# Optimization experiments

Hardware: AMD Instinct MI355X
Metric: run time of the kernel (lower is better)

The kernel has to match this reference:

```python
import jax, jax.numpy as jnp
import numpy as np
from jax import lax

R = 3
D = (2 * R + 1) ** 2  # 49 local offsets


def _unfold(x, r):
    # torch F.unfold(kernel=2r+1, padding=r): (B,C,H,W) -> (B, C*K*K, H, W),
    # channel-major (c, ky, kx) ordering, matching conv_general_dilated_patches.
    k = 2 * r + 1
    return lax.conv_general_dilated_patches(
        x, (k, k), (1, 1), [(r, r), (r, r)],
        dimension_numbers=("NCHW", "OIHW", "NCHW"))


def _l2norm(x, eps=1e-12):
    n = jnp.sqrt(jnp.sum(x * x, axis=1, keepdims=True))
    return x / jnp.maximum(n, eps)


def setup_inputs() -> dict:
    key = jax.random.key(0)
    ks = jax.random.split(key, 8)
    B, Cin, Cmid, H, W = 2, 256, 128, 112, 112
    phi_cur = jax.random.normal(ks[0], (B, Cin, H, W), jnp.float32)
    phi_rnd = jax.random.normal(ks[1], (B, Cin, H, W), jnp.float32)
    P_cur = jax.random.normal(ks[2], (B, 3, H, W), jnp.float32)
    P_rnd = jax.random.normal(ks[3], (B, 3, H, W), jnp.float32)
    Wq = jax.random.normal(ks[4], (Cmid, Cin), jnp.float32) * 0.05
    Wk = jax.random.normal(ks[5], (Cmid, Cin), jnp.float32) * 0.05
    Wv = jax.random.normal(ks[6], (D, D), jnp.float32) * 0.1
    bv = jnp.zeros((D,), jnp.float32)
    gamma = jnp.array(1.0, jnp.float32)
    return dict(phi_cur=phi_cur, phi_rnd=phi_rnd, P_cur=P_cur, P_rnd=P_rnd,
                Wq=Wq, Wk=Wk, Wv=Wv, bv=bv, gamma=gamma)


def reference(phi_cur, phi_rnd, P_cur, P_rnd, Wq, Wk, Wv, bv, gamma):
    B, _, H, W = phi_cur.shape
    # 1x1 convs + channel L2 normalize
    q = _l2norm(jnp.einsum('oc,bchw->bohw', Wq, phi_cur))
    k = _l2norm(jnp.einsum('oc,bchw->bohw', Wk, phi_rnd))
    # local cost volume: patches (B, Cmid, D, H, W)
    patches = _unfold(k, R).reshape(B, -1, D, H, W)
    corr = jnp.einsum('bchw,bcdhw->bdhw', q, patches)  # (B,D,H,W)
    vol_corr = jnp.einsum('ed,bdhw->behw', Wv, corr) + bv[None, :, None, None]
    # geometric bias
    Pr = _unfold(P_rnd, R).reshape(B, 3, D, H, W)
    dP = P_cur[:, :, None, :, :] - Pr  # (B,3,D,H,W)
    dz = dP[:, 2]
    dist = jnp.sqrt(jnp.clip(jnp.sum(dP * dP, axis=1), 1e-12, None))
    logits = vol_corr + gamma * (-dist - 0.5 * jnp.abs(dz))
    w = jax.nn.softmax(logits, axis=1)
    off = jnp.arange(-R, R + 1, dtype=w.dtype)
    dY, dX = jnp.meshgrid(off, off, indexing='ij')
    offx = dX.reshape(1, D, 1, 1)
    offy = dY.reshape(1, D, 1, 1)
    du = jnp.sum(w * offx, axis=1, keepdims=True)
    dv = jnp.sum(w * offy, axis=1, keepdims=True)
    conf = jnp.max(w, axis=1, keepdims=True)
    return du, dv, conf
```

## Files before the change

### kernel.cpp

```cpp
#include <hip/hip_runtime.h>
#include <hip/hip_bf16.h>
#include <math.h>

constexpr int B    = 2;
constexpr int CIN  = 256;
constexpr int CMID = 128;
constexpr int H    = 112;
constexpr int W    = 112;
constexpr int HW   = H * W;
constexpr int NPIX = B * HW;
constexpr int RAD  = 3;
constexpr int KS   = 7;
constexpr int DD   = 49;

typedef __attribute__((ext_vector_type(8))) short  short8;
typedef __attribute__((ext_vector_type(4))) float  float4v;

__device__ __forceinline__ unsigned pkbf(float a, float b) {
    __hip_bfloat162 h = __float22bfloat162_rn(make_float2(a, b));
    union { __hip_bfloat162 h2; unsigned u; } c;
    c.h2 = h;
    return c.u;
}

__global__ __launch_bounds__(256) void prep(
    const float* __restrict__ Wq, const float* __restrict__ Wk,
    const float* __restrict__ Wv,
    unsigned short* __restrict__ wqb, unsigned short* __restrict__ wkb,
    float* __restrict__ wvp)
{
    if (blockIdx.x < 64) {
        const int i  = blockIdx.x * 256 + threadIdx.x;
        const int n4 = (CMID * CIN) / 4;
        const float4 v = (i < n4) ? ((const float4*)Wq)[i] : ((const float4*)Wk)[i - n4];
        uint2 r;
        r.x = pkbf(v.x, v.y);
        r.y = pkbf(v.z, v.w);
        if (i < n4) ((uint2*)wqb)[i] = r;
        else        ((uint2*)wkb)[i - n4] = r;
    } else {
        for (int idx = threadIdx.x; idx < DD * 52; idx += 256) {
            const int r = idx / 52, c = idx % 52;
            wvp[idx] = (c < DD) ? Wv[r * DD + c] : 0.f;
        }
    }
}

constexpr int PSTR = 264;

__global__ __launch_bounds__(256, 4) void proj_mfma(
    const float* __restrict__ phi_cur, const float* __restrict__ phi_rnd,
    const unsigned short* __restrict__ wq_bf, const unsigned short* __restrict__ wk_bf,
    unsigned short* __restrict__ q_ws, unsigned short* __restrict__ k_ws)
{
    __shared__ unsigned short pt[64 * PSTR];
    __shared__ float red[4][64];

    const int tid  = threadIdx.x;
    const int lane = tid & 63;
    const int wv   = __builtin_amdgcn_readfirstlane(tid >> 6);
    const int t    = blockIdx.y;

    const float* __restrict__ phi          = t ? phi_rnd : phi_cur;
    const unsigned short* __restrict__ Wbf = t ? wk_bf : wq_bf;
    unsigned short* __restrict__ outp      = t ? k_ws : q_ws;

    const int pgb = blockIdx.x * 64;
    const int b   = pgb / HW;
    const int pim = pgb % HW;
    const float* pbase = phi + (size_t)b * CIN * HW + pim;

#pragma unroll
    for (int pass = 0; pass < 8; ++pass) {
        const int idx = pass * 256 + tid;
        const int cp  = idx >> 4;
        const int pq  = idx & 15;
        const int c0  = cp * 2;
        const int swz = ((pq >> 1) & 3) << 3;
        const float4 va = *(const float4*)(pbase + (size_t)c0 * HW + pq * 4);
        const float4 vb = *(const float4*)(pbase + (size_t)(c0 + 1) * HW + pq * 4);
        const int col = c0 ^ swz;
        *(unsigned*)(pt + (pq * 4 + 0) * PSTR + col) = pkbf(va.x, vb.x);
        *(unsigned*)(pt + (pq * 4 + 1) * PSTR + col) = pkbf(va.y, vb.y);
        *(unsigned*)(pt + (pq * 4 + 2) * PSTR + col) = pkbf(va.z, vb.z);
        *(unsigned*)(pt + (pq * 4 + 3) * PSTR + col) = pkbf(va.w, vb.w);
    }

    __syncthreads();

    const int m = lane & 15, quad = lane >> 4;
    float4v acc[2][4];
#pragma unroll
    for (int ot = 0; ot < 2; ++ot)
#pragma unroll
        for (int nt = 0; nt < 4; ++nt) acc[ot][nt] = (float4v)0.f;

#pragma unroll
    for (int kc = 0; kc < 8; ++kc) {
        const short8 af0 = *(const short8*)(Wbf +
            (size_t)(wv * 32 + m) * CIN + kc * 32 + quad * 8);
        const short8 af1 = *(const short8*)(Wbf +
            (size_t)(wv * 32 + 16 + m) * CIN + kc * 32 + quad * 8);
        short8 bfr[4];
#pragma unroll
        for (int nt = 0; nt < 4; ++nt) {
            const int row = nt * 16 + m;
            const int col = (kc * 32 + quad * 8) ^ (((row >> 3) & 3) << 3);
            bfr[nt] = *(const short8*)(pt + row * PSTR + col);
        }
#pragma unroll
        for (int nt = 0; nt < 4; ++nt) {
            acc[0][nt] = __builtin_amdgcn_mfma_f32_16x16x32_bf16(af0, bfr[nt], acc[0][nt], 0, 0, 0);
            acc[1][nt] = __builtin_amdgcn_mfma_f32_16x16x32_bf16(af1, bfr[nt], acc[1][nt], 0, 0, 0);
        }
    }

#pragma unroll
    for (int nt = 0; nt < 4; ++nt) {
        float ss = 0.f;
#pragma unroll
        for (int ot = 0; ot < 2; ++ot)
#pragma unroll
            for (int r = 0; r < 4; ++r)
                ss = fmaf(acc[ot][nt][r], acc[ot][nt][r], ss);
        ss += __shfl_xor(ss, 16, 64);
        ss += __shfl_xor(ss, 32, 64);
        if (quad == 0) red[wv][nt * 16 + m] = ss;
    }
    __syncthreads();

    float inv[4];
#pragma unroll
    for (int nt = 0; nt < 4; ++nt) {
        const int px = nt * 16 + m;
        const float tot = red[0][px] + red[1][px] + red[2][px] + red[3][px];
        inv[nt] = 1.f / fmaxf(sqrtf(tot), 1e-12f);
    }

#pragma unroll
    for (int nt = 0; nt < 4; ++nt)
#pragma unroll
        for (int ot = 0; ot < 2; ++ot) {
            uint2 st;
            st.x = pkbf(acc[ot][nt][0] * inv[nt], acc[ot][nt][1] * inv[nt]);
            st.y = pkbf(acc[ot][nt][2] * inv[nt], acc[ot][nt][3] * inv[nt]);
            *(uint2*)(outp + (size_t)(pgb + nt * 16 + m) * CMID
                      + wv * 32 + ot * 16 + quad * 4) = st;
        }
}

constexpr int TILE = 16;
constexpr int COLS = TILE + 6;
constexpr int NV   = KS * COLS;
constexpr int KSTR = 136;

__global__ __launch_bounds__(256) void corr_kernel(
    const unsigned short* __restrict__ q_ws, const unsigned short* __restrict__ k_ws,
    const float* __restrict__ P_cur, const float* __restrict__ P_rnd,
    const float* __restrict__ wvp, const float* __restrict__ bv,
    const float* __restrict__ gamma_p, float* __restrict__ out)
{
    __shared__ unsigned short kt[NV * KSTR];
    __shared__ alignas(16) unsigned short qt[TILE * KSTR];
    __shared__ float cs[TILE][52];

    const int tid  = threadIdx.x;
    const int lane = tid & 63;
    const int wv   = __builtin_amdgcn_readfirstlane(tid >> 6);

    const int fid = (blockIdx.z * H + blockIdx.y) * (W / TILE) + blockIdx.x;
    const int swz = (fid & 7) * 196 + (fid >> 3);
    const int b   = swz / (H * (W / TILE));
    const int rem = swz % (H * (W / TILE));
    const int h   = rem / (W / TILE);
    const int w0  = (rem % (W / TILE)) * TILE;

    const int sub  = tid & 15;
    const int vgrp = tid >> 4;
#pragma unroll
    for (int pass = 0; pass < 10; ++pass) {
        const int vi = pass * 16 + vgrp;
        if (vi < NV) {
            const int rr = vi / COLS;
            const int cc = vi % COLS;
            const int hh = h + rr - RAD;
            const int ww = w0 + cc - RAD;
            uint4 v = make_uint4(0, 0, 0, 0);
            if (hh >= 0 && hh < H && ww >= 0 && ww < W)
                v = *(const uint4*)(k_ws + (size_t)(b * HW + hh * W + ww) * CMID + sub * 8);
            *(uint4*)(kt + vi * KSTR + sub * 8) = v;
        }
    }
    {
        const uint4 v = *(const uint4*)(q_ws + (size_t)(b * HW + h * W + w0 + vgrp) * CMID + sub * 8);
        *(uint4*)(qt + vgrp * KSTR + sub * 8) = v;
    }

    const int  ld    = (lane < DD) ? lane : 0;
    const bool valid = (lane < DD);
    float4 wq4[13];
#pragma unroll
    for (int j = 0; j < 13; ++j)
        wq4[j] = *(const float4*)(wvp + ld * 52 + j * 4);
    const float bvv   = bv[ld];
    const float gamma = gamma_p[0];

    __syncthreads();

    if (tid < TILE * 3)
        cs[tid / 3][49 + tid % 3] = 0.f;

    const int m = lane & 15, quad = lane >> 4;
    for (int g = wv; g < 14; g += 4) {
        const int r  = g >> 1;
        const int nt = g & 1;
        const int vi = min(r * COLS + nt * 16 + m, NV - 1);
        float4v acc = (float4v)0.f;
#pragma unroll
        for (int kc = 0; kc < 4; ++kc) {
            const short8 afrag = *(const short8*)(qt + m * KSTR + kc * 32 + quad * 8);
            const short8 bfrag = *(const short8*)(kt + vi * KSTR + kc * 32 + quad * 8);
            acc = __builtin_amdgcn_mfma_f32_16x16x32_bf16(afrag, bfrag, acc, 0, 0, 0);
        }
#pragma unroll
        for (int reg = 0; reg < 4; ++reg) {
            const int p   = quad * 4 + reg;
            const int off = nt * 16 + m - p;
            if (off >= 0 && off <= 6)
                cs[p][r * 7 + off] = acc[reg];
        }
    }
    __syncthreads();
    float* lsf = reinterpret_cast<float*>(qt);

    const int dy = ld / KS - RAD;
    const int dx = ld % KS - RAD;

#pragma unroll
    for (int i = 0; i < 4; ++i) {
        const int pl = wv * 4 + i;

        const int hn = h + dy, wn = w0 + pl + dx;
        const bool inb = valid && hn >= 0 && hn < H && wn >= 0 && wn < W;
        const float* pc = P_cur + (size_t)b * 3 * HW + (h * W + w0 + pl);
        const float cx = pc[0], cy = pc[HW], cz = pc[2 * HW];
        float rx = 0.f, ry = 0.f, rz = 0.f;
        if (inb) {
            const float* pr = P_rnd + (size_t)b * 3 * HW + (hn * W + wn);
            rx = pr[0]; ry = pr[HW]; rz = pr[2 * HW];
        }
        const float dpx = cx - rx, dpy = cy - ry, dpz = cz - rz;
        const float dist = sqrtf(fmaxf(dpx * dpx + dpy * dpy + dpz * dpz, 1e-12f));

        float logit = -INFINITY;
        if (valid) {
            float va0 = bvv, va1 = 0.f;
#pragma unroll
            for (int e4 = 0; e4 < 13; ++e4) {
                const float4 c4 = *(const float4*)&cs[pl][e4 * 4];
                const float4 w4 = wq4[e4];
                if (e4 & 1) {
                    va1 = fmaf(w4.x, c4.x, va1);
                    va1 = fmaf(w4.y, c4.y, va1);
                    va1 = fmaf(w4.z, c4.z, va1);
                    va1 = fmaf(w4.w, c4.w, va1);
                } else {
                    va0 = fmaf(w4.x, c4.x, va0);
                    va0 = fmaf(w4.y, c4.y, va0);
                    va0 = fmaf(w4.z, c4.z, va0);
                    va0 = fmaf(w4.w, c4.w, va0);
                }
            }
            logit = (va0 + va1) + gamma * (-dist - 0.5f * fabsf(dpz));
        }
        lsf[pl * 64 + lane] = logit;
    }

    {
        const int pli = lane >> 4;
        const int dq  = lane & 15;
        const int pl  = wv * 4 + pli;

        const float4 v = ((const float4*)lsf)[pl * 16 + dq];

        float m4 = fmaxf(fmaxf(v.x, v.y), fmaxf(v.z, v.w));
#pragma unroll
        for (int s = 1; s < 16; s <<= 1)
            m4 = fmaxf(m4, __shfl_xor(m4, s, 64));

        const float e0 = __expf(v.x - m4);
        const float e1 = __expf(v.y - m4);
        const float e2 = __expf(v.z - m4);
        const float e3 = __expf(v.w - m4);
        float Z = (e0 + e1) + (e2 + e3);

        const int c0i = dq * 4;
        float dus = 0.f, dvs = 0.f;
        {
            const float ex[4] = { e0, e1, e2, e3 };
#pragma unroll
            for (int j = 0; j < 4; ++j) {
                const int col = c0i + j;
                dus = fmaf(ex[j], (float)(col % KS - RAD), dus);
                dvs = fmaf(ex[j], (float)(col / KS - RAD), dvs);
            }
        }
#pragma unroll
        for (int s = 1; s < 16; s <<= 1) {
            Z   += __shfl_xor(Z,   s, 64);
            dus += __shfl_xor(dus, s, 64);
            dvs += __shfl_xor(dvs, s, 64);
        }

        if (dq == 0) {
            const int pg = b * HW + h * W + w0 + pl;
            const float invZ = 1.f / Z;
            out[pg]            = dus * invZ;
            out[NPIX + pg]     = dvs * invZ;
            out[2 * NPIX + pg] = invZ;
        }
    }
}

extern "C" void kernel_launch(void* const* d_in, const int* in_sizes, int n_in,
                              void* d_out, int out_size, void* d_ws, size_t ws_size,
                              hipStream_t stream)
{
    const float* phi_cur = (const float*)d_in[0];
    const float* phi_rnd = (const float*)d_in[1];
    const float* P_cur   = (const float*)d_in[2];
    const float* P_rnd   = (const float*)d_in[3];
    const float* Wq      = (const float*)d_in[4];
    const float* Wk      = (const float*)d_in[5];
    const float* Wv      = (const float*)d_in[6];
    const float* bv      = (const float*)d_in[7];
    const float* gm      = (const float*)d_in[8];
    float* out = (float*)d_out;

    unsigned short* ws   = (unsigned short*)d_ws;
    unsigned short* q_ws = ws;
    unsigned short* k_ws = q_ws + (size_t)NPIX * CMID;
    unsigned short* wqb  = k_ws + (size_t)NPIX * CMID;
    unsigned short* wkb  = wqb + (size_t)CMID * CIN;
    float*          wvp  = (float*)(wkb + (size_t)CMID * CIN);

    prep<<<dim3(65), 256, 0, stream>>>(Wq, Wk, Wv, wqb, wkb, wvp);

    proj_mfma<<<dim3(NPIX / 64, 2), 256, 0, stream>>>(
        phi_cur, phi_rnd, wqb, wkb, q_ws, k_ws);

    corr_kernel<<<dim3(W / TILE, H, B), 256, 0, stream>>>(
        q_ws, k_ws, P_cur, P_rnd, wvp, bv, gm, out);
}
```

Before: 138.4 us.

## Fuse weight prep into projection kernel, halve pixel tile, hoist geometry loads

Removes the separate prep launch: the projection kernel now reads fp32 Wq/Wk directly, converts them to bf16 in registers with a one-step prefetch, and block 0 pads Wv. The projection pixel tile shrinks from 64 to 32 pixels per block, which doubles the block count and changes the LDS swizzle. In the correlation kernel the geometric bias loads and math move ahead of the MFMA phase so their global loads overlap the shared-memory work. The cost is that each block re-reads and re-converts fp32 weights, giving more global weight traffic and conversion ALU per block. Block 0 also writes wvp with no ordering against the next kernel other than stream order.

```diff
diff --git a/kernel.cpp b/kernel.cpp
--- a/kernel.cpp
+++ b/kernel.cpp
@@ -23,60 +23,40 @@
     return c.u;
 }
 
-__global__ __launch_bounds__(256) void prep(
+constexpr int PIX  = 32;
+constexpr int PSTR = 264;
+
+__global__ __launch_bounds__(256, 4) void proj_mfma(
+    const float* __restrict__ phi_cur, const float* __restrict__ phi_rnd,
     const float* __restrict__ Wq, const float* __restrict__ Wk,
     const float* __restrict__ Wv,
-    unsigned short* __restrict__ wqb, unsigned short* __restrict__ wkb,
+    unsigned short* __restrict__ q_ws, unsigned short* __restrict__ k_ws,
     float* __restrict__ wvp)
 {
-    if (blockIdx.x < 64) {
-        const int i  = blockIdx.x * 256 + threadIdx.x;
-        const int n4 = (CMID * CIN) / 4;
-        const float4 v = (i < n4) ? ((const float4*)Wq)[i] : ((const float4*)Wk)[i - n4];
-        uint2 r;
-        r.x = pkbf(v.x, v.y);
-        r.y = pkbf(v.z, v.w);
-        if (i < n4) ((uint2*)wqb)[i] = r;
-        else        ((uint2*)wkb)[i - n4] = r;
-    } else {
-        for (int idx = threadIdx.x; idx < DD * 52; idx += 256) {
-            const int r = idx / 52, c = idx % 52;
-            wvp[idx] = (c < DD) ? Wv[r * DD + c] : 0.f;
-        }
-    }
-}
-
-constexpr int PSTR = 264;
-
-__global__ __launch_bounds__(256, 4) void proj_mfma(
-    const float* __restrict__ phi_cur, const float* __restrict__ phi_rnd,
-    const unsigned short* __restrict__ wq_bf, const unsigned short* __restrict__ wk_bf,
-    unsigned short* __restrict__ q_ws, unsigned short* __restrict__ k_ws)
-{
-    __shared__ unsigned short pt[64 * PSTR];
-    __shared__ float red[4][64];
+    __shared__ unsigned short pt[PIX * PSTR];
+    __shared__ float red[4][PIX];
 
     const int tid  = threadIdx.x;
     const int lane = tid & 63;
     const int wv   = __builtin_amdgcn_readfirstlane(tid >> 6);
     const int t    = blockIdx.y;
 
-    const float* __restrict__ phi          = t ? phi_rnd : phi_cur;
-    const unsigned short* __restrict__ Wbf = t ? wk_bf : wq_bf;
-    unsigned short* __restrict__ outp      = t ? k_ws : q_ws;
-
-    const int pgb = blockIdx.x * 64;
+    const float* __restrict__ phi = t ? phi_rnd : phi_cur;
+    const float* __restrict__ Wf  = t ? Wk : Wq;
+    unsigned short* __restrict__ outp = t ? k_ws : q_ws;
+
+    const int pgb = blockIdx.x * PIX;
     const int b   = pgb / HW;
     const int pim = pgb % HW;
     const float* pbase = phi + (size_t)b * CIN * HW + pim;
 
 #pragma unroll
-    for (int pass = 0; pass < 8; ++pass) {
+    for (int pass = 0; pass < 4; ++pass) {
         const int idx = pass * 256 + tid;
-        const int cp  = idx >> 4;
-        const int pq  = idx & 15;
+        const int cp  = idx >> 3;
+        const int pq  = idx & 7;
         const int c0  = cp * 2;
-        const int swz = ((pq >> 1) & 3) << 3;
+        const int swz = ((pq >> 1) & 3) << 4;
         const float4 va = *(const float4*)(pbase + (size_t)c0 * HW + pq * 4);
         const float4 vb = *(const float4*)(pbase + (size_t)(c0 + 1) * HW + pq * 4);
         const int col = c0 ^ swz;
@@ -86,37 +66,62 @@
         *(unsigned*)(pt + (pq * 4 + 3) * PSTR + col) = pkbf(va.w, vb.w);
     }
 
+    if (blockIdx.x == 0 && t == 0) {
+        for (int idx = tid; idx < DD * 52; idx += 256) {
+            const int r = idx / 52, c = idx % 52;
+            wvp[idx] = (c < DD) ? Wv[r * DD + c] : 0.f;
+        }
+    }
+
     __syncthreads();
 
     const int m = lane & 15, quad = lane >> 4;
-    float4v acc[2][4];
+    const float* wr0 = Wf + (size_t)(wv * 32 + m) * CIN + quad * 8;
+    const float* wr1 = Wf + (size_t)(wv * 32 + 16 + m) * CIN + quad * 8;
+
+    float4 c0a = *(const float4*)(wr0);
+    float4 c0b = *(const float4*)(wr0 + 4);
+    float4 c1a = *(const float4*)(wr1);
+    float4 c1b = *(const float4*)(wr1 + 4);
+
+    float4v acc[2][2];
 #pragma unroll
     for (int ot = 0; ot < 2; ++ot)
 #pragma unroll
-        for (int nt = 0; nt < 4; ++nt) acc[ot][nt] = (float4v)0.f;
+        for (int nt = 0; nt < 2; ++nt) acc[ot][nt] = (float4v)0.f;
 
 #pragma unroll
     for (int kc = 0; kc < 8; ++kc) {
-        const short8 af0 = *(const short8*)(Wbf +
-            (size_t)(wv * 32 + m) * CIN + kc * 32 + quad * 8);
-        const short8 af1 = *(const short8*)(Wbf +
-            (size_t)(wv * 32 + 16 + m) * CIN + kc * 32 + quad * 8);
-        short8 bfr[4];
-#pragma unroll
-        for (int nt = 0; nt < 4; ++nt) {
+        const int kn = (kc < 7) ? kc + 1 : 7;
+        const float4 n0a = *(const float4*)(wr0 + kn * 32);
+        const float4 n0b = *(const float4*)(wr0 + kn * 32 + 4);
+        const float4 n1a = *(const float4*)(wr1 + kn * 32);
+        const float4 n1b = *(const float4*)(wr1 + kn * 32 + 4);
+
+        short8 bfr[2];
+#pragma unroll
+        for (int nt = 0; nt < 2; ++nt) {
             const int row = nt * 16 + m;
-            const int col = (kc * 32 + quad * 8) ^ (((row >> 3) & 3) << 3);
+            const int col = (kc * 32 + quad * 8) ^ (((row >> 3) & 3) << 4);
             bfr[nt] = *(const short8*)(pt + row * PSTR + col);
         }
-#pragma unroll
-        for (int nt = 0; nt < 4; ++nt) {
-            acc[0][nt] = __builtin_amdgcn_mfma_f32_16x16x32_bf16(af0, bfr[nt], acc[0][nt], 0, 0, 0);
-            acc[1][nt] = __builtin_amdgcn_mfma_f32_16x16x32_bf16(af1, bfr[nt], acc[1][nt], 0, 0, 0);
-        }
-    }
-
-#pragma unroll
-    for (int nt = 0; nt < 4; ++nt) {
+
+        union { short8 s; unsigned u[4]; } a0, a1;
+        a0.u[0] = pkbf(c0a.x, c0a.y); a0.u[1] = pkbf(c0a.z, c0a.w);
+        a0.u[2] = pkbf(c0b.x, c0b.y); a0.u[3] = pkbf(c0b.z, c0b.w);
+        a1.u[0] = pkbf(c1a.x, c1a.y); a1.u[1] = pkbf(c1a.z, c1a.w);
+        a1.u[2] = pkbf(c1b.x, c1b.y); a1.u[3] = pkbf(c1b.z, c1b.w);
+
+#pragma unroll
+        for (int nt = 0; nt < 2; ++nt) {
+            acc[0][nt] = __builtin_amdgcn_mfma_f32_16x16x32_bf16(a0.s, bfr[nt], acc[0][nt], 0, 0, 0);
+            acc[1][nt] = __builtin_amdgcn_mfma_f32_16x16x32_bf16(a1.s, bfr[nt], acc[1][nt], 0, 0, 0);
+        }
+        c0a = n0a; c0b = n0b; c1a = n1a; c1b = n1b;
+    }
+
+#pragma unroll
+    for (int nt = 0; nt < 2; ++nt) {
         float ss = 0.f;
 #pragma unroll
         for (int ot = 0; ot < 2; ++ot)
@@ -129,16 +134,16 @@
     }
     __syncthreads();
 
-    float inv[4];
-#pragma unroll
-    for (int nt = 0; nt < 4; ++nt) {
+    float inv[2];
+#pragma unroll
+    for (int nt = 0; nt < 2; ++nt) {
         const int px = nt * 16 + m;
         const float tot = red[0][px] + red[1][px] + red[2][px] + red[3][px];
         inv[nt] = 1.f / fmaxf(sqrtf(tot), 1e-12f);
     }
 
 #pragma unroll
-    for (int nt = 0; nt < 4; ++nt)
+    for (int nt = 0; nt < 2; ++nt)
 #pragma unroll
         for (int ot = 0; ot < 2; ++ot) {
             uint2 st;
@@ -205,41 +210,12 @@
     const float bvv   = bv[ld];
     const float gamma = gamma_p[0];
 
-    __syncthreads();
-
-    if (tid < TILE * 3)
-        cs[tid / 3][49 + tid % 3] = 0.f;
-
-    const int m = lane & 15, quad = lane >> 4;
-    for (int g = wv; g < 14; g += 4) {
-        const int r  = g >> 1;
-        const int nt = g & 1;
-        const int vi = min(r * COLS + nt * 16 + m, NV - 1);
-        float4v acc = (float4v)0.f;
-#pragma unroll
-        for (int kc = 0; kc < 4; ++kc) {
-            const short8 afrag = *(const short8*)(qt + m * KSTR + kc * 32 + quad * 8);
-            const short8 bfrag = *(const short8*)(kt + vi * KSTR + kc * 32 + quad * 8);
-            acc = __builtin_amdgcn_mfma_f32_16x16x32_bf16(afrag, bfrag, acc, 0, 0, 0);
-        }
-#pragma unroll
-        for (int reg = 0; reg < 4; ++reg) {
-            const int p   = quad * 4 + reg;
-            const int off = nt * 16 + m - p;
-            if (off >= 0 && off <= 6)
-                cs[p][r * 7 + off] = acc[reg];
-        }
-    }
-    __syncthreads();
-    float* lsf = reinterpret_cast<float*>(qt);
-
     const int dy = ld / KS - RAD;
     const int dx = ld % KS - RAD;
-
+    float geo[4];
 #pragma unroll
     for (int i = 0; i < 4; ++i) {
         const int pl = wv * 4 + i;
-
         const int hn = h + dy, wn = w0 + pl + dx;
         const bool inb = valid && hn >= 0 && hn < H && wn >= 0 && wn < W;
         const float* pc = P_cur + (size_t)b * 3 * HW + (h * W + w0 + pl);
@@ -251,7 +227,40 @@
         }
         const float dpx = cx - rx, dpy = cy - ry, dpz = cz - rz;
         const float dist = sqrtf(fmaxf(dpx * dpx + dpy * dpy + dpz * dpz, 1e-12f));
-
+        geo[i] = gamma * (-dist - 0.5f * fabsf(dpz));
+    }
+
+    __syncthreads();
+
+    if (tid < TILE * 3)
+        cs[tid / 3][49 + tid % 3] = 0.f;
+
+    const int m = lane & 15, quad = lane >> 4;
+    for (int g = wv; g < 14; g += 4) {
+        const int r  = g >> 1;
+        const int nt = g & 1;
+        const int vi = min(r * COLS + nt * 16 + m, NV - 1);
+        float4v acc = (float4v)0.f;
+#pragma unroll
+        for (int kc = 0; kc < 4; ++kc) {
+            const short8 afrag = *(const short8*)(qt + m * KSTR + kc * 32 + quad * 8);
+            const short8 bfrag = *(const short8*)(kt + vi * KSTR + kc * 32 + quad * 8);
+            acc = __builtin_amdgcn_mfma_f32_16x16x32_bf16(afrag, bfrag, acc, 0, 0, 0);
+        }
+#pragma unroll
+        for (int reg = 0; reg < 4; ++reg) {
+            const int p   = quad * 4 + reg;
+            const int off = nt * 16 + m - p;
+            if (off >= 0 && off <= 6)
+                cs[p][r * 7 + off] = acc[reg];
+        }
+    }
+    __syncthreads();
+    float* lsf = reinterpret_cast<float*>(qt);
+
+#pragma unroll
+    for (int i = 0; i < 4; ++i) {
+        const int pl = wv * 4 + i;
         float logit = -INFINITY;
         if (valid) {
             float va0 = bvv, va1 = 0.f;
@@ -271,7 +280,7 @@
                     va0 = fmaf(w4.w, c4.w, va0);
                 }
             }
-            logit = (va0 + va1) + gamma * (-dist - 0.5f * fabsf(dpz));
+            logit = (va0 + va1) + geo[i];
         }
         lsf[pl * 64 + lane] = logit;
     }
@@ -340,14 +349,10 @@
     unsigned short* ws   = (unsigned short*)d_ws;
     unsigned short* q_ws = ws;
     unsigned short* k_ws = q_ws + (size_t)NPIX * CMID;
-    unsigned short* wqb  = k_ws + (size_t)NPIX * CMID;
-    unsigned short* wkb  = wqb + (size_t)CMID * CIN;
-    float*          wvp  = (float*)(wkb + (size_t)CMID * CIN);
-
-    prep<<<dim3(65), 256, 0, stream>>>(Wq, Wk, Wv, wqb, wkb, wvp);
-
-    proj_mfma<<<dim3(NPIX / 64, 2), 256, 0, stream>>>(
-        phi_cur, phi_rnd, wqb, wkb, q_ws, k_ws);
+    float*          wvp  = (float*)(k_ws + (size_t)NPIX * CMID);
+
+    proj_mfma<<<dim3(NPIX / PIX, 2), 256, 0, stream>>>(
+        phi_cur, phi_rnd, Wq, Wk, Wv, q_ws, k_ws, wvp);
 
     corr_kernel<<<dim3(W / TILE, H, B), 256, 0, stream>>>(
         q_ws, k_ws, P_cur, P_rnd, wvp, bv, gm, out);
```

Measured after the change: 146.4 us. 5.8% more time.

## Split projection into transpose-to-bf16 pass and register-fed GEMM kernel

Applied to the files above, without the earlier changes.

The fused projection kernel is split in two. The first kernel, which also takes over weight preparation, transposes phi to a pixel-major bf16 workspace. The second kernel is a GEMM in which each wave owns 16 pixels and all 128 output channels, reading operands straight from global memory with software prefetch and doing the L2 norm with shuffles only, no LDS reduction. In corr_kernel the geometric bias loads are moved ahead of the MFMA stage so they overlap with it. This trades an extra global round trip of the bf16 phi (about 25 MB of writes and reads) for less LDS traffic and fewer barriers in the GEMM.

```diff
diff --git a/kernel.cpp b/kernel.cpp
--- a/kernel.cpp
+++ b/kernel.cpp
@@ -23,48 +23,40 @@
     return c.u;
 }
 
-__global__ __launch_bounds__(256) void prep(
+constexpr int PSTR = 264;
+
+__global__ __launch_bounds__(256, 4) void tposer(
+    const float* __restrict__ phi_cur, const float* __restrict__ phi_rnd,
     const float* __restrict__ Wq, const float* __restrict__ Wk,
     const float* __restrict__ Wv,
+    unsigned short* __restrict__ phb,
     unsigned short* __restrict__ wqb, unsigned short* __restrict__ wkb,
     float* __restrict__ wvp)
 {
-    if (blockIdx.x < 64) {
-        const int i  = blockIdx.x * 256 + threadIdx.x;
-        const int n4 = (CMID * CIN) / 4;
-        const float4 v = (i < n4) ? ((const float4*)Wq)[i] : ((const float4*)Wk)[i - n4];
-        uint2 r;
-        r.x = pkbf(v.x, v.y);
-        r.y = pkbf(v.z, v.w);
-        if (i < n4) ((uint2*)wqb)[i] = r;
-        else        ((uint2*)wkb)[i - n4] = r;
-    } else {
-        for (int idx = threadIdx.x; idx < DD * 52; idx += 256) {
-            const int r = idx / 52, c = idx % 52;
-            wvp[idx] = (c < DD) ? Wv[r * DD + c] : 0.f;
-        }
-    }
-}
-
-constexpr int PSTR = 264;
-
-__global__ __launch_bounds__(256, 4) void proj_mfma(
-    const float* __restrict__ phi_cur, const float* __restrict__ phi_rnd,
-    const unsigned short* __restrict__ wq_bf, const unsigned short* __restrict__ wk_bf,
-    unsigned short* __restrict__ q_ws, unsigned short* __restrict__ k_ws)
-{
+    const int tid = threadIdx.x;
+    const int t   = blockIdx.y;
+
+    if (blockIdx.x == NPIX / 64) {
+        const float* __restrict__ Wsrc = t ? Wk : Wq;
+        unsigned short* __restrict__ Wdst = t ? wkb : wqb;
+        for (int i = tid; i < CMID * CIN / 4; i += 256) {
+            const float4 v = ((const float4*)Wsrc)[i];
+            uint2 r;
+            r.x = pkbf(v.x, v.y);
+            r.y = pkbf(v.z, v.w);
+            ((uint2*)Wdst)[i] = r;
+        }
+        if (t == 0)
+            for (int idx = tid; idx < DD * 52; idx += 256) {
+                const int r = idx / 52, c = idx % 52;
+                wvp[idx] = (c < DD) ? Wv[r * DD + c] : 0.f;
+            }
+        return;
+    }
+
     __shared__ unsigned short pt[64 * PSTR];
-    __shared__ float red[4][64];
-
-    const int tid  = threadIdx.x;
-    const int lane = tid & 63;
-    const int wv   = __builtin_amdgcn_readfirstlane(tid >> 6);
-    const int t    = blockIdx.y;
-
-    const float* __restrict__ phi          = t ? phi_rnd : phi_cur;
-    const unsigned short* __restrict__ Wbf = t ? wk_bf : wq_bf;
-    unsigned short* __restrict__ outp      = t ? k_ws : q_ws;
-
+
+    const float* __restrict__ phi = t ? phi_rnd : phi_cur;
     const int pgb = blockIdx.x * 64;
     const int b   = pgb / HW;
     const int pim = pgb % HW;
@@ -88,65 +80,82 @@
 
     __syncthreads();
 
+    const size_t obase = (size_t)t * NPIX * CIN + (size_t)pgb * CIN;
+#pragma unroll
+    for (int it = 0; it < 8; ++it) {
+        const int g   = it * 256 + tid;
+        const int row = g >> 5;
+        const int c4  = g & 31;
+        const int col = (c4 * 8) ^ (((row >> 3) & 3) << 3);
+        const uint4 v = *(const uint4*)(pt + row * PSTR + col);
+        *(uint4*)(phb + obase + (size_t)row * CIN + c4 * 8) = v;
+    }
+}
+
+__global__ __launch_bounds__(256, 4) void proj_gemm(
+    const unsigned short* __restrict__ phb,
+    const unsigned short* __restrict__ wqb, const unsigned short* __restrict__ wkb,
+    unsigned short* __restrict__ q_ws, unsigned short* __restrict__ k_ws)
+{
+    const int tid  = threadIdx.x;
+    const int lane = tid & 63;
+    const int wv   = __builtin_amdgcn_readfirstlane(tid >> 6);
+    const int t    = blockIdx.y;
+
+    const unsigned short* __restrict__ Wb  = t ? wkb : wqb;
+    const unsigned short* __restrict__ src = phb + (size_t)t * NPIX * CIN;
+    unsigned short* __restrict__ outp      = t ? k_ws : q_ws;
+
     const int m = lane & 15, quad = lane >> 4;
-    float4v acc[2][4];
-#pragma unroll
-    for (int ot = 0; ot < 2; ++ot)
-#pragma unroll
-        for (int nt = 0; nt < 4; ++nt) acc[ot][nt] = (float4v)0.f;
+    const int pix0 = blockIdx.x * 64 + wv * 16;
+    const unsigned short* brow = src + (size_t)(pix0 + m) * CIN + quad * 8;
+    const unsigned short* arow = Wb + (size_t)m * CIN + quad * 8;
+
+    float4v acc[8];
+#pragma unroll
+    for (int ot = 0; ot < 8; ++ot) acc[ot] = (float4v)0.f;
+
+    short8 aF[8], bF;
+    bF = *(const short8*)(brow);
+#pragma unroll
+    for (int ot = 0; ot < 8; ++ot)
+        aF[ot] = *(const short8*)(arow + (size_t)ot * 16 * CIN);
 
 #pragma unroll
     for (int kc = 0; kc < 8; ++kc) {
-        const short8 af0 = *(const short8*)(Wbf +
-            (size_t)(wv * 32 + m) * CIN + kc * 32 + quad * 8);
-        const short8 af1 = *(const short8*)(Wbf +
-            (size_t)(wv * 32 + 16 + m) * CIN + kc * 32 + quad * 8);
-        short8 bfr[4];
-#pragma unroll
-        for (int nt = 0; nt < 4; ++nt) {
-            const int row = nt * 16 + m;
-            const int col = (kc * 32 + quad * 8) ^ (((row >> 3) & 3) << 3);
-            bfr[nt] = *(const short8*)(pt + row * PSTR + col);
-        }
-#pragma unroll
-        for (int nt = 0; nt < 4; ++nt) {
-            acc[0][nt] = __builtin_amdgcn_mfma_f32_16x16x32_bf16(af0, bfr[nt], acc[0][nt], 0, 0, 0);
-            acc[1][nt] = __builtin_amdgcn_mfma_f32_16x16x32_bf16(af1, bfr[nt], acc[1][nt], 0, 0, 0);
-        }
-    }
-
-#pragma unroll
-    for (int nt = 0; nt < 4; ++nt) {
-        float ss = 0.f;
-#pragma unroll
-        for (int ot = 0; ot < 2; ++ot)
-#pragma unroll
-            for (int r = 0; r < 4; ++r)
-                ss = fmaf(acc[ot][nt][r], acc[ot][nt][r], ss);
-        ss += __shfl_xor(ss, 16, 64);
-        ss += __shfl_xor(ss, 32, 64);
-        if (quad == 0) red[wv][nt * 16 + m] = ss;
-    }
-    __syncthreads();
-
-    float inv[4];
-#pragma unroll
-    for (int nt = 0; nt < 4; ++nt) {
-        const int px = nt * 16 + m;
-        const float tot = red[0][px] + red[1][px] + red[2][px] + red[3][px];
-        inv[nt] = 1.f / fmaxf(sqrtf(tot), 1e-12f);
-    }
-
-#pragma unroll
-    for (int nt = 0; nt < 4; ++nt)
-#pragma unroll
-        for (int ot = 0; ot < 2; ++ot) {
-            uint2 st;
-            st.x = pkbf(acc[ot][nt][0] * inv[nt], acc[ot][nt][1] * inv[nt]);
-            st.y = pkbf(acc[ot][nt][2] * inv[nt], acc[ot][nt][3] * inv[nt]);
-            *(uint2*)(outp + (size_t)(pgb + nt * 16 + m) * CMID
-                      + wv * 32 + ot * 16 + quad * 4) = st;
-        }
+        const int kn = (kc < 7) ? kc + 1 : 7;
+        short8 aN[8];
+        const short8 bN = *(const short8*)(brow + kn * 32);
+#pragma unroll
+        for (int ot = 0; ot < 8; ++ot)
+            aN[ot] = *(const short8*)(arow + (size_t)ot * 16 * CIN + kn * 32);
+
+#pragma unroll
+        for (int ot = 0; ot < 8; ++ot)
+            acc[ot] = __builtin_amdgcn_mfma_f32_16x16x32_bf16(aF[ot], bF, acc[ot], 0, 0, 0);
+
+        bF = bN;
+#pragma unroll
+        for (int ot = 0; ot < 8; ++ot) aF[ot] = aN[ot];
+    }
+
+    float ss = 0.f;
+#pragma unroll
+    for (int ot = 0; ot < 8; ++ot)
+#pragma unroll
+        for (int r = 0; r < 4; ++r)
+            ss = fmaf(acc[ot][r], acc[ot][r], ss);
+    ss += __shfl_xor(ss, 16, 64);
+    ss += __shfl_xor(ss, 32, 64);
+    const float inv = 1.f / fmaxf(sqrtf(ss), 1e-12f);
+
+#pragma unroll
+    for (int ot = 0; ot < 8; ++ot) {
+        uint2 st;
+        st.x = pkbf(acc[ot][0] * inv, acc[ot][1] * inv);
+        st.y = pkbf(acc[ot][2] * inv, acc[ot][3] * inv);
+        *(uint2*)(outp + (size_t)(pix0 + m) * CMID + ot * 16 + quad * 4) = st;
+    }
 }
 
 constexpr int TILE = 16;
@@ -205,41 +214,12 @@
     const float bvv   = bv[ld];
     const float gamma = gamma_p[0];
 
-    __syncthreads();
-
-    if (tid < TILE * 3)
-        cs[tid / 3][49 + tid % 3] = 0.f;
-
-    const int m = lane & 15, quad = lane >> 4;
-    for (int g = wv; g < 14; g += 4) {
-        const int r  = g >> 1;
-        const int nt = g & 1;
-        const int vi = min(r * COLS + nt * 16 + m, NV - 1);
-        float4v acc = (float4v)0.f;
-#pragma unroll
-        for (int kc = 0; kc < 4; ++kc) {
-            const short8 afrag = *(const short8*)(qt + m * KSTR + kc * 32 + quad * 8);
-            const short8 bfrag = *(const short8*)(kt + vi * KSTR + kc * 32 + quad * 8);
-            acc = __builtin_amdgcn_mfma_f32_16x16x32_bf16(afrag, bfrag, acc, 0, 0, 0);
-        }
-#pragma unroll
-        for (int reg = 0; reg < 4; ++reg) {
-            const int p   = quad * 4 + reg;
-            const int off = nt * 16 + m - p;
-            if (off >= 0 && off <= 6)
-                cs[p][r * 7 + off] = acc[reg];
-        }
-    }
-    __syncthreads();
-    float* lsf = reinterpret_cast<float*>(qt);
-
     const int dy = ld / KS - RAD;
     const int dx = ld % KS - RAD;
-
+    float geo[4];
 #pragma unroll
     for (int i = 0; i < 4; ++i) {
         const int pl = wv * 4 + i;
-
         const int hn = h + dy, wn = w0 + pl + dx;
         const bool inb = valid && hn >= 0 && hn < H && wn >= 0 && wn < W;
         const float* pc = P_cur + (size_t)b * 3 * HW + (h * W + w0 + pl);
@@ -251,7 +231,40 @@
         }
         const float dpx = cx - rx, dpy = cy - ry, dpz = cz - rz;
         const float dist = sqrtf(fmaxf(dpx * dpx + dpy * dpy + dpz * dpz, 1e-12f));
-
+        geo[i] = gamma * (-dist - 0.5f * fabsf(dpz));
+    }
+
+    __syncthreads();
+
+    if (tid < TILE * 3)
+        cs[tid / 3][49 + tid % 3] = 0.f;
+
+    const int m = lane & 15, quad = lane >> 4;
+    for (int g = wv; g < 14; g += 4) {
+        const int r  = g >> 1;
+        const int nt = g & 1;
+        const int vi = min(r * COLS + nt * 16 + m, NV - 1);
+        float4v acc = (float4v)0.f;
+#pragma unroll
+        for (int kc = 0; kc < 4; ++kc) {
+            const short8 afrag = *(const short8*)(qt + m * KSTR + kc * 32 + quad * 8);
+            const short8 bfrag = *(const short8*)(kt + vi * KSTR + kc * 32 + quad * 8);
+            acc = __builtin_amdgcn_mfma_f32_16x16x32_bf16(afrag, bfrag, acc, 0, 0, 0);
+        }
+#pragma unroll
+        for (int reg = 0; reg < 4; ++reg) {
+            const int p   = quad * 4 + reg;
+            const int off = nt * 16 + m - p;
+            if (off >= 0 && off <= 6)
+                cs[p][r * 7 + off] = acc[reg];
+        }
+    }
+    __syncthreads();
+    float* lsf = reinterpret_cast<float*>(qt);
+
+#pragma unroll
+    for (int i = 0; i < 4; ++i) {
+        const int pl = wv * 4 + i;
         float logit = -INFINITY;
         if (valid) {
             float va0 = bvv, va1 = 0.f;
@@ -271,7 +284,7 @@
                     va0 = fmaf(w4.w, c4.w, va0);
                 }
             }
-            logit = (va0 + va1) + gamma * (-dist - 0.5f * fabsf(dpz));
+            logit = (va0 + va1) + geo[i];
         }
         lsf[pl * 64 + lane] = logit;
     }
@@ -340,14 +353,16 @@
     unsigned short* ws   = (unsigned short*)d_ws;
     unsigned short* q_ws = ws;
     unsigned short* k_ws = q_ws + (size_t)NPIX * CMID;
-    unsigned short* wqb  = k_ws + (size_t)NPIX * CMID;
+    unsigned short* phb  = k_ws + (size_t)NPIX * CMID;
+    unsigned short* wqb  = phb + (size_t)2 * NPIX * CIN;
     unsigned short* wkb  = wqb + (size_t)CMID * CIN;
     float*          wvp  = (float*)(wkb + (size_t)CMID * CIN);
 
-    prep<<<dim3(65), 256, 0, stream>>>(Wq, Wk, Wv, wqb, wkb, wvp);
-
-    proj_mfma<<<dim3(NPIX / 64, 2), 256, 0, stream>>>(
-        phi_cur, phi_rnd, wqb, wkb, q_ws, k_ws);
+    tposer<<<dim3(NPIX / 64 + 1, 2), 256, 0, stream>>>(
+        phi_cur, phi_rnd, Wq, Wk, Wv, phb, wqb, wkb, wvp);
+
+    proj_gemm<<<dim3(NPIX / 64, 2), 256, 0, stream>>>(
+        phb, wqb, wkb, q_ws, k_ws);
 
     corr_kernel<<<dim3(W / TILE, H, B), 256, 0, stream>>>(
         q_ws, k_ws, P_cur, P_rnd, wvp, bv, gm, out);
```

Result: slower. 164.0 us (+18.5%).

## Batch global loads in registers to overlap latency in projection and corr kernels

Applied to the files above, without the earlier changes.

In the projection kernel, the weight fragments are preloaded into registers before the phi staging loop. The phi loads are issued in batches of four before converting and storing to LDS, so more loads are in flight at once. In the corr kernel, the K/Q tile loads are held in registers while the geometric bias terms (P_cur/P_rnd reads, distance) are computed, and only then written to LDS, overlapping global latency with independent work. A launch-bounds occupancy hint of 3 is added, and the extra live registers may raise register pressure or cause spills.

```diff
diff --git a/kernel.cpp b/kernel.cpp
--- a/kernel.cpp
+++ b/kernel.cpp
@@ -70,25 +70,45 @@
     const int pim = pgb % HW;
     const float* pbase = phi + (size_t)b * CIN * HW + pim;
 
-#pragma unroll
-    for (int pass = 0; pass < 8; ++pass) {
-        const int idx = pass * 256 + tid;
-        const int cp  = idx >> 4;
-        const int pq  = idx & 15;
-        const int c0  = cp * 2;
-        const int swz = ((pq >> 1) & 3) << 3;
-        const float4 va = *(const float4*)(pbase + (size_t)c0 * HW + pq * 4);
-        const float4 vb = *(const float4*)(pbase + (size_t)(c0 + 1) * HW + pq * 4);
-        const int col = c0 ^ swz;
-        *(unsigned*)(pt + (pq * 4 + 0) * PSTR + col) = pkbf(va.x, vb.x);
-        *(unsigned*)(pt + (pq * 4 + 1) * PSTR + col) = pkbf(va.y, vb.y);
-        *(unsigned*)(pt + (pq * 4 + 2) * PSTR + col) = pkbf(va.z, vb.z);
-        *(unsigned*)(pt + (pq * 4 + 3) * PSTR + col) = pkbf(va.w, vb.w);
+    const int m = lane & 15, quad = lane >> 4;
+
+    short8 af[2][8];
+#pragma unroll
+    for (int ot = 0; ot < 2; ++ot)
+#pragma unroll
+        for (int kc = 0; kc < 8; ++kc)
+            af[ot][kc] = *(const short8*)(Wbf +
+                (size_t)(wv * 32 + ot * 16 + m) * CIN + kc * 32 + quad * 8);
+
+#pragma unroll
+    for (int half = 0; half < 2; ++half) {
+        float4 va[4], vb[4];
+#pragma unroll
+        for (int p = 0; p < 4; ++p) {
+            const int idx = (half * 4 + p) * 256 + tid;
+            const int cp  = idx >> 4;
+            const int pq  = idx & 15;
+            const int c0  = cp * 2;
+            va[p] = *(const float4*)(pbase + (size_t)c0 * HW + pq * 4);
+            vb[p] = *(const float4*)(pbase + (size_t)(c0 + 1) * HW + pq * 4);
+        }
+#pragma unroll
+        for (int p = 0; p < 4; ++p) {
+            const int idx = (half * 4 + p) * 256 + tid;
+            const int cp  = idx >> 4;
+            const int pq  = idx & 15;
+            const int c0  = cp * 2;
+            const int swz = ((pq >> 1) & 3) << 3;
+            const int col = c0 ^ swz;
+            *(unsigned*)(pt + (pq * 4 + 0) * PSTR + col) = pkbf(va[p].x, vb[p].x);
+            *(unsigned*)(pt + (pq * 4 + 1) * PSTR + col) = pkbf(va[p].y, vb[p].y);
+            *(unsigned*)(pt + (pq * 4 + 2) * PSTR + col) = pkbf(va[p].z, vb[p].z);
+            *(unsigned*)(pt + (pq * 4 + 3) * PSTR + col) = pkbf(va[p].w, vb[p].w);
+        }
     }
 
     __syncthreads();
 
-    const int m = lane & 15, quad = lane >> 4;
     float4v acc[2][4];
 #pragma unroll
     for (int ot = 0; ot < 2; ++ot)
@@ -97,10 +117,6 @@
 
 #pragma unroll
     for (int kc = 0; kc < 8; ++kc) {
-        const short8 af0 = *(const short8*)(Wbf +
-            (size_t)(wv * 32 + m) * CIN + kc * 32 + quad * 8);
-        const short8 af1 = *(const short8*)(Wbf +
-            (size_t)(wv * 32 + 16 + m) * CIN + kc * 32 + quad * 8);
         short8 bfr[4];
 #pragma unroll
         for (int nt = 0; nt < 4; ++nt) {
@@ -110,8 +126,8 @@
         }
 #pragma unroll
         for (int nt = 0; nt < 4; ++nt) {
-            acc[0][nt] = __builtin_amdgcn_mfma_f32_16x16x32_bf16(af0, bfr[nt], acc[0][nt], 0, 0, 0);
-            acc[1][nt] = __builtin_amdgcn_mfma_f32_16x16x32_bf16(af1, bfr[nt], acc[1][nt], 0, 0, 0);
+            acc[0][nt] = __builtin_amdgcn_mfma_f32_16x16x32_bf16(af[0][kc], bfr[nt], acc[0][nt], 0, 0, 0);
+            acc[1][nt] = __builtin_amdgcn_mfma_f32_16x16x32_bf16(af[1][kc], bfr[nt], acc[1][nt], 0, 0, 0);
         }
     }
 
@@ -154,7 +170,7 @@
 constexpr int NV   = KS * COLS;
 constexpr int KSTR = 136;
 
-__global__ __launch_bounds__(256) void corr_kernel(
+__global__ __launch_bounds__(256, 3) void corr_kernel(
     const unsigned short* __restrict__ q_ws, const unsigned short* __restrict__ k_ws,
     const float* __restrict__ P_cur, const float* __restrict__ P_rnd,
     const float* __restrict__ wvp, const float* __restrict__ bv,
@@ -177,24 +193,22 @@
 
     const int sub  = tid & 15;
     const int vgrp = tid >> 4;
+    uint4 stv[10];
 #pragma unroll
     for (int pass = 0; pass < 10; ++pass) {
         const int vi = pass * 16 + vgrp;
+        uint4 v = make_uint4(0, 0, 0, 0);
         if (vi < NV) {
             const int rr = vi / COLS;
             const int cc = vi % COLS;
             const int hh = h + rr - RAD;
             const int ww = w0 + cc - RAD;
-            uint4 v = make_uint4(0, 0, 0, 0);
             if (hh >= 0 && hh < H && ww >= 0 && ww < W)
                 v = *(const uint4*)(k_ws + (size_t)(b * HW + hh * W + ww) * CMID + sub * 8);
-            *(uint4*)(kt + vi * KSTR + sub * 8) = v;
-        }
-    }
-    {
-        const uint4 v = *(const uint4*)(q_ws + (size_t)(b * HW + h * W + w0 + vgrp) * CMID + sub * 8);
-        *(uint4*)(qt + vgrp * KSTR + sub * 8) = v;
-    }
+        }
+        stv[pass] = v;
+    }
+    const uint4 qv = *(const uint4*)(q_ws + (size_t)(b * HW + h * W + w0 + vgrp) * CMID + sub * 8);
 
     const int  ld    = (lane < DD) ? lane : 0;
     const bool valid = (lane < DD);
@@ -205,41 +219,12 @@
     const float bvv   = bv[ld];
     const float gamma = gamma_p[0];
 
-    __syncthreads();
-
-    if (tid < TILE * 3)
-        cs[tid / 3][49 + tid % 3] = 0.f;
-
-    const int m = lane & 15, quad = lane >> 4;
-    for (int g = wv; g < 14; g += 4) {
-        const int r  = g >> 1;
-        const int nt = g & 1;
-        const int vi = min(r * COLS + nt * 16 + m, NV - 1);
-        float4v acc = (float4v)0.f;
-#pragma unroll
-        for (int kc = 0; kc < 4; ++kc) {
-            const short8 afrag = *(const short8*)(qt + m * KSTR + kc * 32 + quad * 8);
-            const short8 bfrag = *(const short8*)(kt + vi * KSTR + kc * 32 + quad * 8);
-            acc = __builtin_amdgcn_mfma_f32_16x16x32_bf16(afrag, bfrag, acc, 0, 0, 0);
-        }
-#pragma unroll
-        for (int reg = 0; reg < 4; ++reg) {
-            const int p   = quad * 4 + reg;
-            const int off = nt * 16 + m - p;
-            if (off >= 0 && off <= 6)
-                cs[p][r * 7 + off] = acc[reg];
-        }
-    }
-    __syncthreads();
-    float* lsf = reinterpret_cast<float*>(qt);
-
     const int dy = ld / KS - RAD;
     const int dx = ld % KS - RAD;
-
+    float geo[4];
 #pragma unroll
     for (int i = 0; i < 4; ++i) {
         const int pl = wv * 4 + i;
-
         const int hn = h + dy, wn = w0 + pl + dx;
         const bool inb = valid && hn >= 0 && hn < H && wn >= 0 && wn < W;
         const float* pc = P_cur + (size_t)b * 3 * HW + (h * W + w0 + pl);
@@ -251,7 +236,48 @@
         }
         const float dpx = cx - rx, dpy = cy - ry, dpz = cz - rz;
         const float dist = sqrtf(fmaxf(dpx * dpx + dpy * dpy + dpz * dpz, 1e-12f));
-
+        geo[i] = gamma * (-dist - 0.5f * fabsf(dpz));
+    }
+
+#pragma unroll
+    for (int pass = 0; pass < 10; ++pass) {
+        const int vi = pass * 16 + vgrp;
+        if (vi < NV)
+            *(uint4*)(kt + vi * KSTR + sub * 8) = stv[pass];
+    }
+    *(uint4*)(qt + vgrp * KSTR + sub * 8) = qv;
+
+    __syncthreads();
+
+    if (tid < TILE * 3)
+        cs[tid / 3][49 + tid % 3] = 0.f;
+
+    const int m = lane & 15, quad = lane >> 4;
+    for (int g = wv; g < 14; g += 4) {
+        const int r  = g >> 1;
+        const int nt = g & 1;
+        const int vi = min(r * COLS + nt * 16 + m, NV - 1);
+        float4v acc = (float4v)0.f;
+#pragma unroll
+        for (int kc = 0; kc < 4; ++kc) {
+            const short8 afrag = *(const short8*)(qt + m * KSTR + kc * 32 + quad * 8);
+            const short8 bfrag = *(const short8*)(kt + vi * KSTR + kc * 32 + quad * 8);
+            acc = __builtin_amdgcn_mfma_f32_16x16x32_bf16(afrag, bfrag, acc, 0, 0, 0);
+        }
+#pragma unroll
+        for (int reg = 0; reg < 4; ++reg) {
+            const int p   = quad * 4 + reg;
+            const int off = nt * 16 + m - p;
+            if (off >= 0 && off <= 6)
+                cs[p][r * 7 + off] = acc[reg];
+        }
+    }
+    __syncthreads();
+    float* lsf = reinterpret_cast<float*>(qt);
+
+#pragma unroll
+    for (int i = 0; i < 4; ++i) {
+        const int pl = wv * 4 + i;
         float logit = -INFINITY;
         if (valid) {
             float va0 = bvv, va1 = 0.f;
@@ -271,7 +297,7 @@
                     va0 = fmaf(w4.w, c4.w, va0);
                 }
             }
-            logit = (va0 + va1) + gamma * (-dist - 0.5f * fabsf(dpz));
+            logit = (va0 + va1) + geo[i];
         }
         lsf[pl * 64 + lane] = logit;
     }
```

Measured after the change: 132.4 us. 1.05x faster.
